# Performance work log

Hardware: AMD Instinct MI355X
Metric: run time of the kernel (lower is better)

Reference implementation:

```python
import jax, jax.numpy as jnp
import numpy as np

B, T, D = 4, 1024, 1024   # batch, seq, embed_dim
E, H = 8, 2048            # expert_count, expert_dim

def setup_inputs() -> dict:
    key = jax.random.key(0)
    ks = jax.random.split(key, 6)
    s = 0.02
    return {
        "x": jax.random.normal(ks[0], (B, T, D), dtype=jnp.float32),
        "padding_mask": jnp.zeros((B, T), dtype=bool),
        "gate_w": jax.random.normal(ks[1], (E, D), dtype=jnp.float32) * s,
        "fc1_w": jax.random.normal(ks[2], (E * H, D), dtype=jnp.float32) * s,
        "fc1_b": jax.random.normal(ks[3], (E * H,), dtype=jnp.float32) * s,
        "fc2_w": jax.random.normal(ks[4], (E * D, H), dtype=jnp.float32) * s,
        "fc2_b": jax.random.normal(ks[5], (E * D,), dtype=jnp.float32) * s,
    }

def reference(x, padding_mask, gate_w, fc1_w, fc1_b, fc2_w, fc2_b):
    b, t, d = x.shape
    e = gate_w.shape[0]
    h = fc1_w.shape[0] // e
    xf = x.reshape(b * t, d)                       # (N, D)
    pm = padding_mask.reshape(b * t)               # (N,)

    # --- Top2Gate (fp32) ---
    logits = (xf @ gate_w.T).astype(jnp.float32)   # (N, E)
    gate_value = jax.nn.softmax(logits, axis=-1)
    gate_value = jnp.where(pm[:, None], 0.0, gate_value)
    top2 = jax.lax.top_k(gate_value, 2)[1]         # (N, 2)
    sel1 = jax.nn.one_hot(top2[:, 0], e, dtype=bool)
    sel2 = jax.nn.one_hot(top2[:, 1], e, dtype=bool)
    sel = sel1 | sel2
    gw = jnp.where(sel, gate_value, 0.0)           # (N, E)
    denom = gw.sum(axis=-1, keepdims=True)
    denom = jnp.where(denom == 0, 1.0, denom)
    gate_weights = (gw / denom).astype(x.dtype)
    nt_real = (~pm).sum().astype(jnp.float32)
    top1_counts = (sel1 & ~pm[:, None]).sum(axis=0).astype(jnp.float32)  # (E,)
    lb_loss = e * ((top1_counts / nt_real) * (gate_value.sum(axis=0) / nt_real)).sum()

    # --- dense per-expert FFN ---
    a = jax.nn.relu(xf @ fc1_w.T + fc1_b)          # (N, E*H)
    a = a.reshape(-1, e, h)                        # (N, E, H)
    w2 = fc2_w.reshape(e, d, h)                    # (E, D, H)
    b2 = fc2_b.reshape(e, d)                       # (E, D)
    y = jnp.einsum('beh,edh->bed', a, w2) + b2     # (N, E, D)
    out = (y * gate_weights[:, :, None]).sum(axis=1).reshape(b, t, d)
    return out, gate_value.reshape(b, t, e), lb_loss
```

## Files before the change

kernel.cpp:

```cpp
#include <hip/hip_runtime.h>

#define NTOK 4096
#define DIM  1024
#define NEXP 8
#define HDIM 2048
#define CAP  9216

typedef unsigned short u16;
typedef __attribute__((ext_vector_type(8))) __bf16 bf16x8;
typedef __attribute__((ext_vector_type(4))) float  f32x4;
typedef __attribute__((ext_vector_type(8))) u16    u16x8;

__device__ inline u16 f2bf(float f) {
    union { float f; unsigned u; } v; v.f = f;
    unsigned r = v.u + 0x7fff + ((v.u >> 16) & 1);
    return (u16)(r >> 16);
}

__device__ inline void gload_lds16(const void* g, void* l) {
    __builtin_amdgcn_global_load_lds(
        (const __attribute__((address_space(1))) unsigned int*)g,
        (__attribute__((address_space(3))) unsigned int*)l, 16, 0, 0);
}

__global__ __launch_bounds__(256) void cvt_kernel(const float* __restrict__ in,
                                                  u16* __restrict__ out, int n8) {
    int stride = gridDim.x * 256;
    for (int i = blockIdx.x * 256 + threadIdx.x; i < n8; i += stride) {
        float4 a = ((const float4*)in)[(size_t)i * 2];
        float4 b = ((const float4*)in)[(size_t)i * 2 + 1];
        u16x8 v;
        v[0]=f2bf(a.x); v[1]=f2bf(a.y); v[2]=f2bf(a.z); v[3]=f2bf(a.w);
        v[4]=f2bf(b.x); v[5]=f2bf(b.y); v[6]=f2bf(b.z); v[7]=f2bf(b.w);
        ((u16x8*)out)[i] = v;
    }
}

__global__ __launch_bounds__(256) void gate_kernel(
    const float* __restrict__ x, const unsigned char* __restrict__ pm,
    const float* __restrict__ gw, float* __restrict__ gate_out,
    int* __restrict__ tok_e, float* __restrict__ tok_w,
    int* __restrict__ counts, float* __restrict__ gv_sum,
    float* __restrict__ top1c, float* __restrict__ nt_acc) {
    __shared__ float lgw[NEXP * DIM];
    __shared__ float bgv[NEXP];
    __shared__ float bt1[NEXP];
    __shared__ int   bcnt[NEXP];
    __shared__ float bnt;
    int t = threadIdx.x;
    for (int k = t; k < NEXP * DIM / 4; k += 256)
        ((float4*)lgw)[k] = ((const float4*)gw)[k];
    if (t < NEXP) { bgv[t] = 0.f; bt1[t] = 0.f; bcnt[t] = 0; }
    if (t == 0) bnt = 0.f;
    __syncthreads();

    int lane = t & 63, wv = t >> 6;
    for (int i = 0; i < 4; ++i) {
        int tok = blockIdx.x * 16 + wv * 4 + i;
        float acc[NEXP];
#pragma unroll
        for (int e = 0; e < NEXP; ++e) acc[e] = 0.f;
        const float* xr = x + (size_t)tok * DIM;
        for (int j = lane; j < DIM; j += 64) {
            float xv = xr[j];
#pragma unroll
            for (int e = 0; e < NEXP; ++e) acc[e] += xv * lgw[e * DIM + j];
        }
#pragma unroll
        for (int e = 0; e < NEXP; ++e) {
            float s = acc[e];
            for (int off = 1; off < 64; off <<= 1) s += __shfl_xor(s, off);
            acc[e] = s;
        }
        if (lane == 0) {
            bool padded = pm[tok] != 0;
            float m = acc[0];
            for (int e = 1; e < NEXP; ++e) m = fmaxf(m, acc[e]);
            float ex[NEXP]; float ssum = 0.f;
            for (int e = 0; e < NEXP; ++e) { ex[e] = expf(acc[e] - m); ssum += ex[e]; }
            float inv = 1.f / ssum;
            float gv[NEXP];
            for (int e = 0; e < NEXP; ++e) gv[e] = padded ? 0.f : ex[e] * inv;
            for (int e = 0; e < NEXP; ++e) gate_out[(size_t)tok * NEXP + e] = gv[e];
            int t1 = 0;
            for (int e = 1; e < NEXP; ++e) if (gv[e] > gv[t1]) t1 = e;
            int t2 = (t1 == 0) ? 1 : 0;
            for (int e = 0; e < NEXP; ++e) { if (e == t1 || e == t2) continue; if (gv[e] > gv[t2]) t2 = e; }
            float w1 = gv[t1], w2 = gv[t2], den = w1 + w2;
            float invd = (den > 0.f) ? 1.f / den : 0.f;
            tok_e[tok * 2]     = t1;  tok_e[tok * 2 + 1] = t2;
            tok_w[tok * 2]     = w1 * invd;
            tok_w[tok * 2 + 1] = w2 * invd;
            atomicAdd(&bcnt[t1], 1); atomicAdd(&bcnt[t2], 1);
            if (!padded) {
                atomicAdd(&bt1[t1], 1.f); atomicAdd(&bnt, 1.f);
                for (int e = 0; e < NEXP; ++e) atomicAdd(&bgv[e], gv[e]);
            }
        }
    }
    __syncthreads();
    if (t < NEXP) {
        atomicAdd(&counts[t], bcnt[t]);
        atomicAdd(&gv_sum[t], bgv[t]);
        atomicAdd(&top1c[t],  bt1[t]);
    }
    if (t == 0) atomicAdd(nt_acc, bnt);
}

__global__ void scan_kernel(const int* __restrict__ counts, int* __restrict__ offsets) {
    if (threadIdx.x == 0 && blockIdx.x == 0) {
        int o = 0;
        for (int e = 0; e < NEXP; ++e) { offsets[e] = o; o += (counts[e] + 127) & ~127; }
        offsets[NEXP] = o;
    }
}

__global__ __launch_bounds__(256) void scatter_kernel(
    const int* __restrict__ tok_e, const float* __restrict__ tok_w,
    const int* __restrict__ offsets, int* __restrict__ fill,
    int* __restrict__ tokens_l, float* __restrict__ gatew_l) {
    int tok = blockIdx.x * 256 + threadIdx.x;
    if (tok >= NTOK) return;
    for (int k = 0; k < 2; ++k) {
        int e = tok_e[tok * 2 + k];
        int p = atomicAdd(&fill[e], 1);
        int pos = offsets[e] + p;
        tokens_l[pos] = tok;
        gatew_l[pos]  = tok_w[tok * 2 + k];
    }
}

template <int EPI, int KDIM, int NDIM, int ASTRIDE>
__global__ __launch_bounds__(256, 2) void gemm_kernel(
    const u16* __restrict__ A, const u16* __restrict__ Bw,
    const float* __restrict__ bias,
    const int* __restrict__ tokens_l, const float* __restrict__ gatew_l,
    const int* __restrict__ counts, const int* __restrict__ offsets,
    u16* __restrict__ actout, float* __restrict__ out) {
    int e = blockIdx.z;
    int count = counts[e];
    int tm = blockIdx.y;
    if (tm * 128 >= count) return;
    int tn = blockIdx.x;
    int offs = offsets[e];

    __shared__ __align__(16) u16 lA[128 * 64];
    __shared__ __align__(16) u16 lB[128 * 64];

    int t = threadIdx.x, lane = t & 63;
    const u16* Ap[4]; const u16* Bp[4];
#pragma unroll
    for (int it = 0; it < 4; ++it) {
        int f = it * 256 + t;
        int row = f >> 3, c8 = f & 7;
        size_t arow;
        if (EPI == 1) arow = (size_t)tokens_l[offs + tm * 128 + row];
        else          arow = (size_t)(offs + tm * 128 + row);
        Ap[it] = A + arow * ASTRIDE + c8 * 8;
        Bp[it] = Bw + ((size_t)e * NDIM + tn * 128 + row) * KDIM + c8 * 8;
    }

    f32x4 acc[4][4];
#pragma unroll
    for (int i = 0; i < 4; ++i)
#pragma unroll
        for (int j = 0; j < 4; ++j) acc[i][j] = (f32x4)(0.f);

    int wm = (t >> 6) >> 1, wn = (t >> 6) & 1;
    int l16 = lane & 15, lq = lane >> 4;

    for (int kt = 0; kt < KDIM / 64; ++kt) {
#pragma unroll
        for (int it = 0; it < 4; ++it) {
            gload_lds16(Ap[it] + kt * 64, &lA[(it * 256 + t) * 8]);
            gload_lds16(Bp[it] + kt * 64, &lB[(it * 256 + t) * 8]);
        }
        asm volatile("s_waitcnt vmcnt(0)" ::: "memory");
        __syncthreads();
#pragma unroll
        for (int kk = 0; kk < 2; ++kk) {
            bf16x8 av[4], bv[4];
#pragma unroll
            for (int mi = 0; mi < 4; ++mi)
                av[mi] = *(const bf16x8*)&lA[(wm * 64 + mi * 16 + l16) * 64 + kk * 32 + lq * 8];
#pragma unroll
            for (int ni = 0; ni < 4; ++ni)
                bv[ni] = *(const bf16x8*)&lB[(wn * 64 + ni * 16 + l16) * 64 + kk * 32 + lq * 8];
#pragma unroll
            for (int mi = 0; mi < 4; ++mi)
#pragma unroll
                for (int ni = 0; ni < 4; ++ni)
                    acc[mi][ni] = __builtin_amdgcn_mfma_f32_16x16x32_bf16(av[mi], bv[ni], acc[mi][ni], 0, 0, 0);
        }
        __syncthreads();
    }

    if (EPI == 1) {
#pragma unroll
        for (int ni = 0; ni < 4; ++ni) {
            int gcol = tn * 128 + wn * 64 + ni * 16 + l16;
            float bv_ = bias[e * NDIM + gcol];
#pragma unroll
            for (int mi = 0; mi < 4; ++mi)
#pragma unroll
                for (int r = 0; r < 4; ++r) {
                    int grow = tm * 128 + wm * 64 + mi * 16 + lq * 4 + r;
                    float v = acc[mi][ni][r] + bv_;
                    v = fmaxf(v, 0.f);
                    actout[(size_t)(offs + grow) * HDIM + gcol] = f2bf(v);
                }
        }
    } else {
#pragma unroll
        for (int mi = 0; mi < 4; ++mi)
#pragma unroll
            for (int r = 0; r < 4; ++r) {
                int grow = tm * 128 + wm * 64 + mi * 16 + lq * 4 + r;
                if (grow < count) {
                    int   tk = tokens_l[offs + grow];
                    float w  = gatew_l[offs + grow];
#pragma unroll
                    for (int ni = 0; ni < 4; ++ni) {
                        int gcol = tn * 128 + wn * 64 + ni * 16 + l16;
                        float v = (acc[mi][ni][r] + bias[e * NDIM + gcol]) * w;
                        atomicAdd(&out[(size_t)tk * DIM + gcol], v);
                    }
                }
            }
    }
}

__global__ void loss_kernel(const float* __restrict__ gv_sum, const float* __restrict__ top1c,
                            const float* __restrict__ nt_acc, float* __restrict__ lout) {
    if (threadIdx.x == 0 && blockIdx.x == 0) {
        float nt = nt_acc[0];
        if (nt <= 0.f) nt = 1.f;
        float s = 0.f;
        for (int e = 0; e < NEXP; ++e) s += top1c[e] * gv_sum[e];
        lout[0] = NEXP * s / (nt * nt);
    }
}

extern "C" void kernel_launch(void* const* d_in, const int* in_sizes, int n_in,
                              void* d_out, int out_size, void* d_ws, size_t ws_size,
                              hipStream_t stream) {
    const float* x      = (const float*)d_in[0];
    const unsigned char* pm = (const unsigned char*)d_in[1];
    const float* gate_w = (const float*)d_in[2];
    const float* fc1_w  = (const float*)d_in[3];
    const float* fc1_b  = (const float*)d_in[4];
    const float* fc2_w  = (const float*)d_in[5];
    const float* fc2_b  = (const float*)d_in[6];

    float* out      = (float*)d_out;
    float* gate_out = out + (size_t)NTOK * DIM;
    float* loss_out = gate_out + (size_t)NTOK * NEXP;

    char* ws = (char*)d_ws;
    int*   counts   = (int*)ws;
    int*   fill     = counts + 8;
    float* gv_sum   = (float*)(ws + 64);
    float* top1c    = (float*)(ws + 96);
    float* nt_acc   = (float*)(ws + 128);
    int*   offsets  = (int*)(ws + 160);
    int*   tokens_l = (int*)(ws + 256);
    float* gatew_l  = (float*)(ws + 256 + CAP * 4);
    int*   tok_e    = (int*)(ws + 256 + CAP * 8);
    float* tok_w    = (float*)(ws + 256 + CAP * 8 + NTOK * 8);
    size_t off = 256 + (size_t)CAP * 8 + (size_t)NTOK * 16;
    u16* x_bf  = (u16*)(ws + off); off += (size_t)NTOK * DIM * 2;
    u16* w1_bf = (u16*)(ws + off); off += (size_t)NEXP * HDIM * DIM * 2;
    u16* w2_bf = (u16*)(ws + off); off += (size_t)NEXP * DIM * HDIM * 2;
    u16* act   = (u16*)(ws + off); off += (size_t)CAP * HDIM * 2;

    hipMemsetAsync(ws, 0, 256 + (size_t)CAP * 8, stream);
    hipMemsetAsync(d_out, 0, (size_t)NTOK * DIM * 4, stream);

    cvt_kernel<<<2048, 256, 0, stream>>>(x,     x_bf,  NTOK * DIM / 8);
    cvt_kernel<<<4096, 256, 0, stream>>>(fc1_w, w1_bf, NEXP * HDIM * DIM / 8);
    cvt_kernel<<<4096, 256, 0, stream>>>(fc2_w, w2_bf, NEXP * DIM * HDIM / 8);

    gate_kernel<<<256, 256, 0, stream>>>(x, pm, gate_w, gate_out, tok_e, tok_w,
                                         counts, gv_sum, top1c, nt_acc);
    scan_kernel<<<1, 64, 0, stream>>>(counts, offsets);
    scatter_kernel<<<16, 256, 0, stream>>>(tok_e, tok_w, offsets, fill, tokens_l, gatew_l);

    dim3 g1(16, 32, NEXP);
    gemm_kernel<1, 1024, 2048, 1024><<<g1, 256, 0, stream>>>(
        x_bf, w1_bf, fc1_b, tokens_l, gatew_l, counts, offsets, act, nullptr);
    dim3 g2(8, 32, NEXP);
    gemm_kernel<2, 2048, 1024, 2048><<<g2, 256, 0, stream>>>(
        act, w2_bf, fc2_b, tokens_l, gatew_l, counts, offsets, nullptr, out);

    loss_kernel<<<1, 64, 0, stream>>>(gv_sum, top1c, nt_acc, loss_out);
}
```

Measured before the change: 419.4 us.

## Triple-buffer expert GEMMs with swizzled LDS, bigger tiles, and atomic-free combine

The expert GEMMs now use 512-thread blocks with 256x128 tiles. They keep three LDS stages in flight with partial vmcnt waits and raw barriers, and XOR-swizzle the LDS columns to cut bank conflicts. Expert index moves into blockIdx.x so experts interleave across the grid. The second GEMM writes gate-weighted rows to a staging buffer instead of doing fp32 atomics into the output, and a new combine kernel sums each token's two expert rows through a recorded position map. The three convert launches become one, the loss is folded into the scan kernel, and the output memset is dropped. The tradeoffs are a large per-block LDS footprint, extra staging traffic for the combine step, and reuse of the bf16 x and fc1 workspace for the staging buffer.

```diff
diff --git a/kernel.cpp b/kernel.cpp
--- a/kernel.cpp
+++ b/kernel.cpp
@@ -4,7 +4,7 @@
 #define DIM  1024
 #define NEXP 8
 #define HDIM 2048
-#define CAP  9216
+#define CAP  10240
 
 typedef unsigned short u16;
 typedef __attribute__((ext_vector_type(8))) __bf16 bf16x8;
@@ -23,16 +23,25 @@
         (__attribute__((address_space(3))) unsigned int*)l, 16, 0, 0);
 }
 
-__global__ __launch_bounds__(256) void cvt_kernel(const float* __restrict__ in,
-                                                  u16* __restrict__ out, int n8) {
+__global__ __launch_bounds__(256) void cvt_all_kernel(
+    const float* __restrict__ x, const float* __restrict__ w1, const float* __restrict__ w2,
+    u16* __restrict__ x_bf, u16* __restrict__ w1_bf, u16* __restrict__ w2_bf) {
+    const int C0 = NTOK * DIM / 8;
+    const int C1 = NEXP * HDIM * DIM / 8;
+    const int C2 = NEXP * DIM * HDIM / 8;
+    int total = C0 + C1 + C2;
     int stride = gridDim.x * 256;
-    for (int i = blockIdx.x * 256 + threadIdx.x; i < n8; i += stride) {
-        float4 a = ((const float4*)in)[(size_t)i * 2];
-        float4 b = ((const float4*)in)[(size_t)i * 2 + 1];
+    for (int i = blockIdx.x * 256 + threadIdx.x; i < total; i += stride) {
+        const float* src; u16* dst; int j;
+        if (i < C0)            { src = x;  dst = x_bf;  j = i; }
+        else if (i < C0 + C1)  { src = w1; dst = w1_bf; j = i - C0; }
+        else                   { src = w2; dst = w2_bf; j = i - C0 - C1; }
+        float4 a = ((const float4*)src)[(size_t)j * 2];
+        float4 b = ((const float4*)src)[(size_t)j * 2 + 1];
         u16x8 v;
         v[0]=f2bf(a.x); v[1]=f2bf(a.y); v[2]=f2bf(a.z); v[3]=f2bf(a.w);
         v[4]=f2bf(b.x); v[5]=f2bf(b.y); v[6]=f2bf(b.z); v[7]=f2bf(b.w);
-        ((u16x8*)out)[i] = v;
+        ((u16x8*)dst)[j] = v;
     }
 }
 
@@ -107,18 +116,25 @@
     if (t == 0) atomicAdd(nt_acc, bnt);
 }
 
-__global__ void scan_kernel(const int* __restrict__ counts, int* __restrict__ offsets) {
+__global__ void scan_loss_kernel(const int* __restrict__ counts, int* __restrict__ offsets,
+                                 const float* __restrict__ gv_sum, const float* __restrict__ top1c,
+                                 const float* __restrict__ nt_acc, float* __restrict__ lout) {
     if (threadIdx.x == 0 && blockIdx.x == 0) {
         int o = 0;
-        for (int e = 0; e < NEXP; ++e) { offsets[e] = o; o += (counts[e] + 127) & ~127; }
+        for (int e = 0; e < NEXP; ++e) { offsets[e] = o; o += (counts[e] + 255) & ~255; }
         offsets[NEXP] = o;
+        float nt = nt_acc[0];
+        if (nt <= 0.f) nt = 1.f;
+        float s = 0.f;
+        for (int e = 0; e < NEXP; ++e) s += top1c[e] * gv_sum[e];
+        lout[0] = NEXP * s / (nt * nt);
     }
 }
 
 __global__ __launch_bounds__(256) void scatter_kernel(
     const int* __restrict__ tok_e, const float* __restrict__ tok_w,
     const int* __restrict__ offsets, int* __restrict__ fill,
-    int* __restrict__ tokens_l, float* __restrict__ gatew_l) {
+    int* __restrict__ tokens_l, float* __restrict__ gatew_l, int* __restrict__ pos_of) {
     int tok = blockIdx.x * 256 + threadIdx.x;
     if (tok >= NTOK) return;
     for (int k = 0; k < 2; ++k) {
@@ -127,37 +143,41 @@
         int pos = offsets[e] + p;
         tokens_l[pos] = tok;
         gatew_l[pos]  = tok_w[tok * 2 + k];
+        pos_of[tok * 2 + k] = pos;
     }
 }
 
 template <int EPI, int KDIM, int NDIM, int ASTRIDE>
-__global__ __launch_bounds__(256, 2) void gemm_kernel(
+__global__ __launch_bounds__(512, 2) void gemm_kernel(
     const u16* __restrict__ A, const u16* __restrict__ Bw,
     const float* __restrict__ bias,
     const int* __restrict__ tokens_l, const float* __restrict__ gatew_l,
     const int* __restrict__ counts, const int* __restrict__ offsets,
-    u16* __restrict__ actout, float* __restrict__ out) {
-    int e = blockIdx.z;
+    u16* __restrict__ actout, float* __restrict__ yout) {
+    int e  = blockIdx.x & 7;
+    int tn = blockIdx.x >> 3;
+    int tm = blockIdx.y;
     int count = counts[e];
-    int tm = blockIdx.y;
-    if (tm * 128 >= count) return;
-    int tn = blockIdx.x;
+    if (tm * 256 >= count) return;
     int offs = offsets[e];
 
-    __shared__ __align__(16) u16 lA[128 * 64];
-    __shared__ __align__(16) u16 lB[128 * 64];
-
-    int t = threadIdx.x, lane = t & 63;
-    const u16* Ap[4]; const u16* Bp[4];
-#pragma unroll
-    for (int it = 0; it < 4; ++it) {
-        int f = it * 256 + t;
-        int row = f >> 3, c8 = f & 7;
-        size_t arow;
-        if (EPI == 1) arow = (size_t)tokens_l[offs + tm * 128 + row];
-        else          arow = (size_t)(offs + tm * 128 + row);
-        Ap[it] = A + arow * ASTRIDE + c8 * 8;
-        Bp[it] = Bw + ((size_t)e * NDIM + tn * 128 + row) * KDIM + c8 * 8;
+    __shared__ __align__(16) u16 lds[3 * 24576];
+
+    int t = threadIdx.x;
+    int tr8 = t >> 3, c8 = t & 7;
+    int sc8 = c8 ^ (tr8 & 7);
+    const u16* Ap[4]; const u16* Bp[2];
+#pragma unroll
+    for (int l = 0; l < 4; ++l) {
+        int row = l * 64 + tr8;
+        size_t arow = (EPI == 1) ? (size_t)tokens_l[offs + tm * 256 + row]
+                                 : (size_t)(offs + tm * 256 + row);
+        Ap[l] = A + arow * ASTRIDE + sc8 * 8;
+    }
+#pragma unroll
+    for (int l = 0; l < 2; ++l) {
+        int row = l * 64 + tr8;
+        Bp[l] = Bw + ((size_t)e * NDIM + tn * 128 + row) * (size_t)KDIM + sc8 * 8;
     }
 
     f32x4 acc[4][4];
@@ -166,48 +186,74 @@
 #pragma unroll
         for (int j = 0; j < 4; ++j) acc[i][j] = (f32x4)(0.f);
 
-    int wm = (t >> 6) >> 1, wn = (t >> 6) & 1;
-    int l16 = lane & 15, lq = lane >> 4;
-
-    for (int kt = 0; kt < KDIM / 64; ++kt) {
-#pragma unroll
-        for (int it = 0; it < 4; ++it) {
-            gload_lds16(Ap[it] + kt * 64, &lA[(it * 256 + t) * 8]);
-            gload_lds16(Bp[it] + kt * 64, &lB[(it * 256 + t) * 8]);
-        }
-        asm volatile("s_waitcnt vmcnt(0)" ::: "memory");
-        __syncthreads();
+    int lane = t & 63, w = t >> 6;
+    int wr = w >> 1, wc = w & 1;
+    int l16 = lane & 15, lq = lane >> 4, rx = l16 & 7;
+
+    auto STAGE = [&](int kt, int buf) {
+        u16* b0 = &lds[buf * 24576];
+#pragma unroll
+        for (int l = 0; l < 4; ++l)
+            gload_lds16(Ap[l] + kt * 64, b0 + (l * 512 + t) * 8);
+#pragma unroll
+        for (int l = 0; l < 2; ++l)
+            gload_lds16(Bp[l] + kt * 64, b0 + 16384 + (l * 512 + t) * 8);
+    };
+
+    const int NKT = KDIM / 64;
+    STAGE(0, 0);
+    STAGE(1, 1);
+
+    int cb = 0, sb = 2;
+#pragma unroll 1
+    for (int kt = 0; kt < NKT; ++kt) {
+        if (kt + 2 < NKT) {
+            STAGE(kt + 2, sb);
+            sb = (sb == 2) ? 0 : sb + 1;
+            asm volatile("s_waitcnt vmcnt(12)" ::: "memory");
+        } else if (kt + 1 < NKT) {
+            asm volatile("s_waitcnt vmcnt(6)" ::: "memory");
+        } else {
+            asm volatile("s_waitcnt vmcnt(0)" ::: "memory");
+        }
+        __builtin_amdgcn_s_barrier();
+        asm volatile("" ::: "memory");
+        const u16* LA = &lds[cb * 24576];
+        const u16* LB = &lds[cb * 24576 + 16384];
+        __builtin_amdgcn_s_setprio(1);
 #pragma unroll
         for (int kk = 0; kk < 2; ++kk) {
             bf16x8 av[4], bv[4];
 #pragma unroll
             for (int mi = 0; mi < 4; ++mi)
-                av[mi] = *(const bf16x8*)&lA[(wm * 64 + mi * 16 + l16) * 64 + kk * 32 + lq * 8];
+                av[mi] = *(const bf16x8*)&LA[(wr * 64 + mi * 16 + l16) * 64 + (((kk * 4 + lq) ^ rx) * 8)];
 #pragma unroll
             for (int ni = 0; ni < 4; ++ni)
-                bv[ni] = *(const bf16x8*)&lB[(wn * 64 + ni * 16 + l16) * 64 + kk * 32 + lq * 8];
+                bv[ni] = *(const bf16x8*)&LB[(wc * 64 + ni * 16 + l16) * 64 + (((kk * 4 + lq) ^ rx) * 8)];
 #pragma unroll
             for (int mi = 0; mi < 4; ++mi)
 #pragma unroll
                 for (int ni = 0; ni < 4; ++ni)
                     acc[mi][ni] = __builtin_amdgcn_mfma_f32_16x16x32_bf16(av[mi], bv[ni], acc[mi][ni], 0, 0, 0);
         }
-        __syncthreads();
+        __builtin_amdgcn_s_setprio(0);
+        asm volatile("" ::: "memory");
+        __builtin_amdgcn_s_barrier();
+        asm volatile("" ::: "memory");
+        cb = (cb == 2) ? 0 : cb + 1;
     }
 
     if (EPI == 1) {
 #pragma unroll
         for (int ni = 0; ni < 4; ++ni) {
-            int gcol = tn * 128 + wn * 64 + ni * 16 + l16;
-            float bv_ = bias[e * NDIM + gcol];
+            int col = tn * 128 + wc * 64 + ni * 16 + l16;
+            float bb = bias[e * NDIM + col];
 #pragma unroll
             for (int mi = 0; mi < 4; ++mi)
 #pragma unroll
                 for (int r = 0; r < 4; ++r) {
-                    int grow = tm * 128 + wm * 64 + mi * 16 + lq * 4 + r;
-                    float v = acc[mi][ni][r] + bv_;
-                    v = fmaxf(v, 0.f);
-                    actout[(size_t)(offs + grow) * HDIM + gcol] = f2bf(v);
+                    int row = tm * 256 + wr * 64 + mi * 16 + lq * 4 + r;
+                    actout[(size_t)(offs + row) * HDIM + col] = f2bf(fmaxf(acc[mi][ni][r] + bb, 0.f));
                 }
         }
     } else {
@@ -215,29 +261,28 @@
         for (int mi = 0; mi < 4; ++mi)
 #pragma unroll
             for (int r = 0; r < 4; ++r) {
-                int grow = tm * 128 + wm * 64 + mi * 16 + lq * 4 + r;
-                if (grow < count) {
-                    int   tk = tokens_l[offs + grow];
-                    float w  = gatew_l[offs + grow];
-#pragma unroll
-                    for (int ni = 0; ni < 4; ++ni) {
-                        int gcol = tn * 128 + wn * 64 + ni * 16 + l16;
-                        float v = (acc[mi][ni][r] + bias[e * NDIM + gcol]) * w;
-                        atomicAdd(&out[(size_t)tk * DIM + gcol], v);
-                    }
+                int row = tm * 256 + wr * 64 + mi * 16 + lq * 4 + r;
+                float gw_ = gatew_l[offs + row];
+#pragma unroll
+                for (int ni = 0; ni < 4; ++ni) {
+                    int col = tn * 128 + wc * 64 + ni * 16 + l16;
+                    yout[(size_t)(offs + row) * NDIM + col] = (acc[mi][ni][r] + bias[e * NDIM + col]) * gw_;
                 }
             }
     }
 }
 
-__global__ void loss_kernel(const float* __restrict__ gv_sum, const float* __restrict__ top1c,
-                            const float* __restrict__ nt_acc, float* __restrict__ lout) {
-    if (threadIdx.x == 0 && blockIdx.x == 0) {
-        float nt = nt_acc[0];
-        if (nt <= 0.f) nt = 1.f;
-        float s = 0.f;
-        for (int e = 0; e < NEXP; ++e) s += top1c[e] * gv_sum[e];
-        lout[0] = NEXP * s / (nt * nt);
+__global__ __launch_bounds__(256) void combine_kernel(
+    const float* __restrict__ y, const int* __restrict__ pos_of, float* __restrict__ out) {
+    int stride = gridDim.x * 256;
+    for (int idx = blockIdx.x * 256 + threadIdx.x; idx < NTOK * DIM / 4; idx += stride) {
+        int tok = idx >> 8;
+        int c4  = idx & 255;
+        int p1 = pos_of[tok * 2], p2 = pos_of[tok * 2 + 1];
+        float4 a = ((const float4*)y)[(size_t)p1 * 256 + c4];
+        float4 b = ((const float4*)y)[(size_t)p2 * 256 + c4];
+        float4 o; o.x = a.x + b.x; o.y = a.y + b.y; o.z = a.z + b.z; o.w = a.w + b.w;
+        ((float4*)out)[idx] = o;
     }
 }
 
@@ -258,7 +303,7 @@
 
     char* ws = (char*)d_ws;
     int*   counts   = (int*)ws;
-    int*   fill     = counts + 8;
+    int*   fill     = (int*)(ws + 32);
     float* gv_sum   = (float*)(ws + 64);
     float* top1c    = (float*)(ws + 96);
     float* nt_acc   = (float*)(ws + 128);
@@ -267,30 +312,31 @@
     float* gatew_l  = (float*)(ws + 256 + CAP * 4);
     int*   tok_e    = (int*)(ws + 256 + CAP * 8);
     float* tok_w    = (float*)(ws + 256 + CAP * 8 + NTOK * 8);
-    size_t off = 256 + (size_t)CAP * 8 + (size_t)NTOK * 16;
-    u16* x_bf  = (u16*)(ws + off); off += (size_t)NTOK * DIM * 2;
+    int*   pos_of   = (int*)(ws + 256 + CAP * 8 + NTOK * 16);
+    size_t off = 256 + (size_t)CAP * 8 + (size_t)NTOK * 24;
+    u16* x_bf  = (u16*)(ws + off);
+    float* y_part = (float*)(ws + off);
+    off += (size_t)NTOK * DIM * 2;
     u16* w1_bf = (u16*)(ws + off); off += (size_t)NEXP * HDIM * DIM * 2;
     u16* w2_bf = (u16*)(ws + off); off += (size_t)NEXP * DIM * HDIM * 2;
     u16* act   = (u16*)(ws + off); off += (size_t)CAP * HDIM * 2;
 
     hipMemsetAsync(ws, 0, 256 + (size_t)CAP * 8, stream);
-    hipMemsetAsync(d_out, 0, (size_t)NTOK * DIM * 4, stream);
-
-    cvt_kernel<<<2048, 256, 0, stream>>>(x,     x_bf,  NTOK * DIM / 8);
-    cvt_kernel<<<4096, 256, 0, stream>>>(fc1_w, w1_bf, NEXP * HDIM * DIM / 8);
-    cvt_kernel<<<4096, 256, 0, stream>>>(fc2_w, w2_bf, NEXP * DIM * HDIM / 8);
+
+    cvt_all_kernel<<<2048, 256, 0, stream>>>(x, fc1_w, fc2_w, x_bf, w1_bf, w2_bf);
 
     gate_kernel<<<256, 256, 0, stream>>>(x, pm, gate_w, gate_out, tok_e, tok_w,
                                          counts, gv_sum, top1c, nt_acc);
-    scan_kernel<<<1, 64, 0, stream>>>(counts, offsets);
-    scatter_kernel<<<16, 256, 0, stream>>>(tok_e, tok_w, offsets, fill, tokens_l, gatew_l);
-
-    dim3 g1(16, 32, NEXP);
-    gemm_kernel<1, 1024, 2048, 1024><<<g1, 256, 0, stream>>>(
+    scan_loss_kernel<<<1, 64, 0, stream>>>(counts, offsets, gv_sum, top1c, nt_acc, loss_out);
+    scatter_kernel<<<16, 256, 0, stream>>>(tok_e, tok_w, offsets, fill,
+                                           tokens_l, gatew_l, pos_of);
+
+    dim3 g1(8 * 16, 8);
+    gemm_kernel<1, 1024, 2048, 1024><<<g1, 512, 0, stream>>>(
         x_bf, w1_bf, fc1_b, tokens_l, gatew_l, counts, offsets, act, nullptr);
-    dim3 g2(8, 32, NEXP);
-    gemm_kernel<2, 2048, 1024, 2048><<<g2, 256, 0, stream>>>(
-        act, w2_bf, fc2_b, tokens_l, gatew_l, counts, offsets, nullptr, out);
-
-    loss_kernel<<<1, 64, 0, stream>>>(gv_sum, top1c, nt_acc, loss_out);
-}
+    dim3 g2(8 * 8, 8);
+    gemm_kernel<2, 2048, 1024, 2048><<<g2, 512, 0, stream>>>(
+        act, w2_bf, fc2_b, tokens_l, gatew_l, counts, offsets, nullptr, y_part);
+
+    combine_kernel<<<2048, 256, 0, stream>>>(y_part, pos_of, out);
+}
```

Result: faster. 394.6 us (-5.9%).
